# Kernel optimization log

Measured on AMD Instinct MI355X. Metric: run time of the kernel, lower is better.

The kernel has to match this reference:

```python
import jax, jax.numpy as jnp
import numpy as np

PAD = 4          # pad_size == max_displacement
K = 1            # avgpool kernel_size
S1, S2 = 1, 1    # avgpool strides


def _avg_pool(x, k, s1, s2):
    # x: [B, C, H, W]; AvgPool2d(k, stride=(s1, s2)) with VALID padding
    if k == 1 and s1 == 1 and s2 == 1:
        return x
    summed = jax.lax.reduce_window(
        x, 0.0, jax.lax.add,
        window_dimensions=(1, 1, k, k),
        window_strides=(1, 1, s1, s2),
        padding='VALID')
    return summed / float(k * k)


def setup_inputs() -> dict:
    key = jax.random.key(0)
    k1, k2 = jax.random.split(key)
    shape = (8, 196, 128, 224)
    input1 = jax.random.normal(k1, shape, dtype=jnp.float32)
    input2 = jax.random.normal(k2, shape, dtype=jnp.float32)
    return {"input1": input1, "input2": input2}


def reference(input1, input2):
    B, C, H, W = input1.shape
    # reflect-pad input2 spatially by PAD on each side
    x2 = jnp.pad(input2, ((0, 0), (0, 0), (PAD, PAD), (PAD, PAD)), mode='reflect')
    corrs = []
    for hi in range(2 * PAD + 1):        # fixed small displacement set (9x9)
        for wi in range(2 * PAD + 1):
            shifted = jax.lax.dynamic_slice(x2, (0, 0, hi, wi), (B, C, H, W))
            prod = input1 * shifted                      # [B,C,H,W]
            pooled = _avg_pool(prod, K, S1, S2)          # [B,C,H',W']
            corrs.append(jnp.sum(pooled, axis=1) / C)    # [B,H',W']
    return jnp.stack(corrs, axis=1)                      # [B,81,H',W']
```

## Files before the change

### kernel.cpp

```cpp
#include <hip/hip_runtime.h>


constexpr int NB = 8, NC = 196, NH = 128, NW = 224;
constexpr int ND = 9;
constexpr int PADV = 4;
constexpr int WS = 232;
constexpr int KC = 2;
constexpr int NSLOT = 56;
constexpr int ACTIVE = ND * NSLOT;
constexpr int TPB = 512;
constexpr int HWSZ = NH * NW;

__device__ __forceinline__ int refl(int v, int n) {
    v = v < 0 ? -v : v;
    return v >= n ? 2 * n - 2 - v : v;
}

__global__ __launch_bounds__(TPB)
void corr_kernel(const float* __restrict__ in1,
                 const float* __restrict__ in2,
                 float* __restrict__ out)
{
    __shared__ float s_win[KC][ND][WS];

    const int tid = threadIdx.x;
    const int bh  = blockIdx.x;
    const int b   = bh / NH;
    const int h   = bh - b * NH;

    const float* gA[2];
    int  lA[2];
    bool vA[2];
#pragma unroll
    for (int k = 0; k < 2; ++k) {
        int v  = tid + k * TPB;
        vA[k]  = v < KC * ND * NSLOT;
        int vv = vA[k] ? v : 0;
        int cc = vv / (ND * NSLOT);
        int r  = vv - cc * (ND * NSLOT);
        int dh = r / NSLOT;
        int g  = r - dh * NSLOT;
        int y  = refl(h + dh - PADV, NH);
        gA[k]  = in2 + ((b * NC + cc) * NH + y) * NW + 4 * g;
        lA[k]  = (cc * ND + dh) * WS + 4 + 4 * g;
    }
    const float* gB = in2;
    int  lB = 0;
    const bool vB = tid < KC * ND * 8;
    {
        int v  = vB ? tid : 0;
        int cc = v / (ND * 8);
        int r  = v - cc * (ND * 8);
        int dh = r / 8;
        int e  = r - dh * 8;
        int s  = e < 4 ? e : 224 + e;
        int x  = e < 4 ? 4 - e : 226 - e;
        int y  = refl(h + dh - PADV, NH);
        gB = in2 + ((b * NC + cc) * NH + y) * NW + x;
        lB = (cc * ND + dh) * WS + s;
    }

    const int  cdh  = tid / NSLOT;
    const int  slot = tid - cdh * NSLOT;
    const int  w0   = slot * 4;
    const bool compute = tid < ACTIVE;
    const float* a1p = in1 + ((b * NC) * NH + h) * NW + w0;

    float acc[ND][4];
#pragma unroll
    for (int d = 0; d < ND; ++d)
#pragma unroll
        for (int p = 0; p < 4; ++p) acc[d][p] = 0.f;

    float4 bufA[2];
    float  bufB = 0.f;
#pragma unroll
    for (int k = 0; k < 2; ++k)
        if (vA[k]) bufA[k] = *(const float4*)(gA[k]);
    if (vB) bufB = gB[0];

    for (int c0 = 0; c0 < NC; c0 += KC) {
        __syncthreads();
#pragma unroll
        for (int k = 0; k < 2; ++k)
            if (vA[k]) *(float4*)&((float*)s_win)[lA[k]] = bufA[k];
        if (vB) ((float*)s_win)[lB] = bufB;
        __syncthreads();

        const int c1 = c0 + KC;
        if (c1 < NC) {
            const int off = c1 * HWSZ;
#pragma unroll
            for (int k = 0; k < 2; ++k)
                if (vA[k]) bufA[k] = *(const float4*)(gA[k] + off);
            if (vB) bufB = gB[off];
        }

        if (compute) {
#pragma unroll
            for (int cc = 0; cc < KC; ++cc) {
                const float* wrow = &s_win[cc][cdh][w0];
                float4 wv0 = *(const float4*)(wrow);
                float4 wv1 = *(const float4*)(wrow + 4);
                float4 wv2 = *(const float4*)(wrow + 8);
                const float wn[12] = {wv0.x, wv0.y, wv0.z, wv0.w,
                                      wv1.x, wv1.y, wv1.z, wv1.w,
                                      wv2.x, wv2.y, wv2.z, wv2.w};
                float4 a = *(const float4*)(a1p + (c0 + cc) * HWSZ);
#pragma unroll
                for (int d = 0; d < ND; ++d) {
                    acc[d][0] += a.x * wn[d + 0];
                    acc[d][1] += a.y * wn[d + 1];
                    acc[d][2] += a.z * wn[d + 2];
                    acc[d][3] += a.w * wn[d + 3];
                }
            }
        }
    }

    if (compute) {
        const float scale = 1.0f / 196.0f;
#pragma unroll
        for (int d = 0; d < ND; ++d) {
            float4 o;
            o.x = acc[d][0] * scale;
            o.y = acc[d][1] * scale;
            o.z = acc[d][2] * scale;
            o.w = acc[d][3] * scale;
            float* op = out + (((b * (ND * ND)) + cdh * ND + d) * NH + h) * NW + w0;
            *(float4*)op = o;
        }
    }
}

extern "C" void kernel_launch(void* const* d_in, const int* in_sizes, int n_in,
                              void* d_out, int out_size, void* d_ws, size_t ws_size,
                              hipStream_t stream)
{
    const float* in1 = (const float*)d_in[0];
    const float* in2 = (const float*)d_in[1];
    float* outp = (float*)d_out;
    dim3 grid(NB * NH);
    dim3 block(TPB);
    hipLaunchKernelGGL(corr_kernel, grid, block, 0, stream, in1, in2, outp);
}
```

Baseline: 657.1 us.

## Double-buffer the shared window and prefetch input1 to halve barriers per round

Turns the single shared-memory window into a ping-pong pair of buffers. The loop now processes two channel-pair rounds per iteration, with one barrier per round instead of two. It also prefetches the input1 registers one round ahead, so global loads overlap with the FMA work. The row stride is padded from 232 to 236 floats, which changes the LDS bank mapping. The cost is twice the shared memory and more live registers, which could reduce occupancy.

```diff
diff --git a/kernel.cpp b/kernel.cpp
--- a/kernel.cpp
+++ b/kernel.cpp
@@ -4,12 +4,14 @@
 constexpr int NB = 8, NC = 196, NH = 128, NW = 224;
 constexpr int ND = 9;
 constexpr int PADV = 4;
-constexpr int WS = 232;
+constexpr int WSP = 236;
 constexpr int KC = 2;
 constexpr int NSLOT = 56;
 constexpr int ACTIVE = ND * NSLOT;
 constexpr int TPB = 512;
 constexpr int HWSZ = NH * NW;
+constexpr int NROUND = NC / KC;
+constexpr int BUF = KC * ND * WSP;
 
 __device__ __forceinline__ int refl(int v, int n) {
     v = v < 0 ? -v : v;
@@ -21,7 +23,7 @@
                  const float* __restrict__ in2,
                  float* __restrict__ out)
 {
-    __shared__ float s_win[KC][ND][WS];
+    __shared__ __align__(16) float s_win[2 * BUF];
 
     const int tid = threadIdx.x;
     const int bh  = blockIdx.x;
@@ -42,7 +44,7 @@
         int g  = r - dh * NSLOT;
         int y  = refl(h + dh - PADV, NH);
         gA[k]  = in2 + ((b * NC + cc) * NH + y) * NW + 4 * g;
-        lA[k]  = (cc * ND + dh) * WS + 4 + 4 * g;
+        lA[k]  = (cc * ND + dh) * WSP + 4 + 4 * g;
     }
     const float* gB = in2;
     int  lB = 0;
@@ -57,7 +59,7 @@
         int x  = e < 4 ? 4 - e : 226 - e;
         int y  = refl(h + dh - PADV, NH);
         gB = in2 + ((b * NC + cc) * NH + y) * NW + x;
-        lB = (cc * ND + dh) * WS + s;
+        lB = (cc * ND + dh) * WSP + s;
     }
 
     const int  cdh  = tid / NSLOT;
@@ -72,50 +74,88 @@
 #pragma unroll
         for (int p = 0; p < 4; ++p) acc[d][p] = 0.f;
 
-    float4 bufA[2];
-    float  bufB = 0.f;
+    float4 sA[2];
+    float  sB = 0.f;
 #pragma unroll
     for (int k = 0; k < 2; ++k)
-        if (vA[k]) bufA[k] = *(const float4*)(gA[k]);
-    if (vB) bufB = gB[0];
+        if (vA[k]) sA[k] = *(const float4*)(gA[k]);
+    if (vB) sB = gB[0];
+#pragma unroll
+    for (int k = 0; k < 2; ++k)
+        if (vA[k]) *(float4*)&s_win[lA[k]] = sA[k];
+    if (vB) s_win[lB] = sB;
+#pragma unroll
+    for (int k = 0; k < 2; ++k)
+        if (vA[k]) sA[k] = *(const float4*)(gA[k] + KC * HWSZ);
+    if (vB) sB = gB[KC * HWSZ];
+    float4 iE[2], iO[2];
+    if (compute) {
+        iE[0] = *(const float4*)(a1p + 0 * HWSZ);
+        iE[1] = *(const float4*)(a1p + 1 * HWSZ);
+    }
+    __syncthreads();
 
-    for (int c0 = 0; c0 < NC; c0 += KC) {
-        __syncthreads();
+    auto do_compute = [&](const float* base, const float4* iv) {
+#pragma unroll
+        for (int cc = 0; cc < KC; ++cc) {
+            const float* wrow = base + (cc * ND + cdh) * WSP + w0;
+            float4 wv0 = *(const float4*)(wrow);
+            float4 wv1 = *(const float4*)(wrow + 4);
+            float4 wv2 = *(const float4*)(wrow + 8);
+            const float wn[12] = {wv0.x, wv0.y, wv0.z, wv0.w,
+                                  wv1.x, wv1.y, wv1.z, wv1.w,
+                                  wv2.x, wv2.y, wv2.z, wv2.w};
+            const float4 a = iv[cc];
+#pragma unroll
+            for (int d = 0; d < ND; ++d) {
+                acc[d][0] += a.x * wn[d + 0];
+                acc[d][1] += a.y * wn[d + 1];
+                acc[d][2] += a.z * wn[d + 2];
+                acc[d][3] += a.w * wn[d + 3];
+            }
+        }
+    };
+
+    for (int r = 0; r < NROUND; r += 2) {
 #pragma unroll
         for (int k = 0; k < 2; ++k)
-            if (vA[k]) *(float4*)&((float*)s_win)[lA[k]] = bufA[k];
-        if (vB) ((float*)s_win)[lB] = bufB;
+            if (vA[k]) *(float4*)&s_win[BUF + lA[k]] = sA[k];
+        if (vB) s_win[BUF + lB] = sB;
+        if (r + 2 < NROUND) {
+            const int off = (r + 2) * KC * HWSZ;
+#pragma unroll
+            for (int k = 0; k < 2; ++k)
+                if (vA[k]) sA[k] = *(const float4*)(gA[k] + off);
+            if (vB) sB = gB[off];
+        }
+        if (compute) {
+            const int c = (r + 1) * KC;
+            iO[0] = *(const float4*)(a1p + (c + 0) * HWSZ);
+            iO[1] = *(const float4*)(a1p + (c + 1) * HWSZ);
+        }
+        do_compute(&s_win[0], iE);
         __syncthreads();
 
-        const int c1 = c0 + KC;
-        if (c1 < NC) {
-            const int off = c1 * HWSZ;
+        if (r + 2 < NROUND) {
 #pragma unroll
             for (int k = 0; k < 2; ++k)
-                if (vA[k]) bufA[k] = *(const float4*)(gA[k] + off);
-            if (vB) bufB = gB[off];
-        }
-
-        if (compute) {
+                if (vA[k]) *(float4*)&s_win[lA[k]] = sA[k];
+            if (vB) s_win[lB] = sB;
+            if (r + 3 < NROUND) {
+                const int off = (r + 3) * KC * HWSZ;
 #pragma unroll
-            for (int cc = 0; cc < KC; ++cc) {
-                const float* wrow = &s_win[cc][cdh][w0];
-                float4 wv0 = *(const float4*)(wrow);
-                float4 wv1 = *(const float4*)(wrow + 4);
-                float4 wv2 = *(const float4*)(wrow + 8);
-                const float wn[12] = {wv0.x, wv0.y, wv0.z, wv0.w,
-                                      wv1.x, wv1.y, wv1.z, wv1.w,
-                                      wv2.x, wv2.y, wv2.z, wv2.w};
-                float4 a = *(const float4*)(a1p + (c0 + cc) * HWSZ);
-#pragma unroll
-                for (int d = 0; d < ND; ++d) {
-                    acc[d][0] += a.x * wn[d + 0];
-                    acc[d][1] += a.y * wn[d + 1];
-                    acc[d][2] += a.z * wn[d + 2];
-                    acc[d][3] += a.w * wn[d + 3];
-                }
+                for (int k = 0; k < 2; ++k)
+                    if (vA[k]) sA[k] = *(const float4*)(gA[k] + off);
+                if (vB) sB = gB[off];
+            }
+            if (compute) {
+                const int c = (r + 2) * KC;
+                iE[0] = *(const float4*)(a1p + (c + 0) * HWSZ);
+                iE[1] = *(const float4*)(a1p + (c + 1) * HWSZ);
             }
         }
+        do_compute(&s_win[BUF], iO);
+        __syncthreads();
     }
 
     if (compute) {
```

Result: slower. 868.0 us (+32.1%).
